# Kernel tuning notes

Hardware: AMD Instinct MI355X
Metric: run time of the kernel (lower is better)

Reference implementation:

```python
import jax, jax.numpy as jnp
import numpy as np

N_EMBD = 1024
N_HEAD = 16
B, T = 4, 2048

def setup_inputs() -> dict:
    key = jax.random.key(0)
    ks = jax.random.split(key, 5)
    s = 0.02
    return {
        "x": jax.random.normal(ks[0], (B, T, N_EMBD), dtype=jnp.float32),
        "w_attn": jax.random.normal(ks[1], (N_EMBD, 3 * N_EMBD), dtype=jnp.float32) * s,
        "b_attn": jnp.zeros((3 * N_EMBD,), dtype=jnp.float32),
        "w_proj": jax.random.normal(ks[2], (N_EMBD, N_EMBD), dtype=jnp.float32) * s,
        "b_proj": jnp.zeros((N_EMBD,), dtype=jnp.float32),
    }

def reference(x, w_attn, b_attn, w_proj, b_proj):
    Bx, Tx, C = x.shape
    hd = C // N_HEAD
    qkv = x @ w_attn + b_attn  # [B,T,3C]
    q, k, v = jnp.split(qkv, 3, axis=-1)
    # [B,H,T,hd]
    q = q.reshape(Bx, Tx, N_HEAD, hd).transpose(0, 2, 1, 3)
    k = k.reshape(Bx, Tx, N_HEAD, hd).transpose(0, 2, 1, 3)
    v = v.reshape(Bx, Tx, N_HEAD, hd).transpose(0, 2, 1, 3)
    scale = 1.0 / np.sqrt(hd).astype(np.float32)
    wei = jnp.einsum('bhqd,bhkd->bhqk', q, k) * scale
    causal = jnp.tril(jnp.ones((Tx, Tx), dtype=bool))
    wei = jnp.where(causal[None, None], wei, jnp.float32(-jnp.inf))
    wei = jax.nn.softmax(wei, axis=-1)
    out = jnp.einsum('bhqk,bhkd->bhqd', wei, v)
    out = out.transpose(0, 2, 1, 3).reshape(Bx, Tx, C)
    return out @ w_proj + b_proj
```

## Files before the change

kernel.cpp:

```cpp
#include <hip/hip_runtime.h>
#include <hip/hip_bf16.h>
#include <math.h>

#define BB 4
#define TT 2048
#define CC 1024
#define HH 16
#define HD 64
#define C3 3072
#define MM (BB * TT)

typedef __attribute__((ext_vector_type(8))) short bf16x8;
typedef __attribute__((ext_vector_type(4))) float f32x4;
typedef __attribute__((ext_vector_type(4))) short s16x4;

__device__ inline short f32_to_bf16_bits(float f) {
    unsigned u = __float_as_uint(f);
    u += 0x7fffu + ((u >> 16) & 1u);
    return (short)(u >> 16);
}

__device__ inline void async_copy16(const void* g, void* l) {
    __builtin_amdgcn_global_load_lds((const __attribute__((address_space(1))) void*)g,
                                     (__attribute__((address_space(3))) void*)l, 16, 0, 0);
}

__global__ __launch_bounds__(256) void cast_x(const float* __restrict__ in,
                                              short* __restrict__ out) {
    int i = (blockIdx.x * 256 + threadIdx.x) * 8;
    float4 a = *(const float4*)(in + i);
    float4 b = *(const float4*)(in + i + 4);
    bf16x8 o;
    o[0] = f32_to_bf16_bits(a.x); o[1] = f32_to_bf16_bits(a.y);
    o[2] = f32_to_bf16_bits(a.z); o[3] = f32_to_bf16_bits(a.w);
    o[4] = f32_to_bf16_bits(b.x); o[5] = f32_to_bf16_bits(b.y);
    o[6] = f32_to_bf16_bits(b.z); o[7] = f32_to_bf16_bits(b.w);
    *(bf16x8*)(out + i) = o;
}

__global__ __launch_bounds__(256) void tcast(const float* __restrict__ w,
                                             short* __restrict__ wt,
                                             int K, int N) {
    __shared__ short tile[64][68];
    const int n0 = blockIdx.x * 64, k0 = blockIdx.y * 64;
    const int tid = threadIdx.x;
#pragma unroll
    for (int it = 0; it < 4; ++it) {
        int idx = it * 1024 + tid * 4;
        int r = idx >> 6, c = idx & 63;
        float4 v = *(const float4*)&w[(size_t)(k0 + r) * N + n0 + c];
        tile[r][c + 0] = f32_to_bf16_bits(v.x);
        tile[r][c + 1] = f32_to_bf16_bits(v.y);
        tile[r][c + 2] = f32_to_bf16_bits(v.z);
        tile[r][c + 3] = f32_to_bf16_bits(v.w);
    }
    __syncthreads();
#pragma unroll
    for (int it = 0; it < 4; ++it) {
        int idx = it * 256 + tid;
        int rr = idx >> 4, kc = (idx & 15) * 4;
        s16x4 o = { tile[kc + 0][rr], tile[kc + 1][rr], tile[kc + 2][rr], tile[kc + 3][rr] };
        *(s16x4*)&wt[(size_t)(n0 + rr) * K + k0 + kc] = o;
    }
}

template <bool QKV>
__global__ __launch_bounds__(256) void gemm128(const short* __restrict__ A,
                                               const short* __restrict__ Bt,
                                               const float* __restrict__ bias,
                                               short* __restrict__ qb,
                                               short* __restrict__ kb,
                                               short* __restrict__ vt,
                                               float* __restrict__ out,
                                               int N, int Kdim) {
    __shared__ __align__(16) short As[128 * 64];
    __shared__ __align__(16) short Bs[128 * 64];
    const int tid = threadIdx.x;
    const int wave = tid >> 6, lane = tid & 63;
    const int quad = lane >> 4, l16 = lane & 15;
    const int wm = wave >> 1, wn = wave & 1;

    const int nbx = gridDim.x;
    const int cpc = nbx >> 3;
    const int id = blockIdx.y * nbx + blockIdx.x;
    const int cls = id & 7;
    const int rr = id >> 3;
    const int n_idx = cls * cpc + rr % cpc;
    const int m_idx = rr / cpc;
    const int m0 = m_idx * 128, n0 = n_idx * 128;

    f32x4 acc[4][4] = {};

    for (int k0 = 0; k0 < Kdim; k0 += 64) {
#pragma unroll
        for (int c2 = 0; c2 < 4; ++c2) {
            int g = (wave * 4 + c2) * 64 + lane;
            int row = g >> 3;
            int seg = (g & 7) ^ (row & 7);
            async_copy16(A + (size_t)(m0 + row) * Kdim + k0 + seg * 8, As + g * 8);
            async_copy16(Bt + (size_t)(n0 + row) * Kdim + k0 + seg * 8, Bs + g * 8);
        }
        __syncthreads();
#pragma unroll
        for (int ks = 0; ks < 2; ++ks) {
            bf16x8 af[4], bfv[4];
#pragma unroll
            for (int i = 0; i < 4; ++i) {
                int row = wm * 64 + i * 16 + l16;
                int u = (ks * 4 + quad) ^ (row & 7);
                af[i] = *(const bf16x8*)&As[row * 64 + u * 8];
            }
#pragma unroll
            for (int j = 0; j < 4; ++j) {
                int row = wn * 64 + j * 16 + l16;
                int u = (ks * 4 + quad) ^ (row & 7);
                bfv[j] = *(const bf16x8*)&Bs[row * 64 + u * 8];
            }
#pragma unroll
            for (int i = 0; i < 4; ++i)
#pragma unroll
                for (int j = 0; j < 4; ++j)
                    acc[i][j] = __builtin_amdgcn_mfma_f32_16x16x32_bf16(af[i], bfv[j], acc[i][j], 0, 0, 0);
        }
        __syncthreads();
    }

#pragma unroll
    for (int i = 0; i < 4; ++i)
#pragma unroll
        for (int j = 0; j < 4; ++j) {
            int n = n0 + wn * 64 + j * 16 + l16;
            float bv = bias[n];
            if (QKV) {
                int which = n >> 10, cc = n & 1023;
                int h = cc >> 6, d = cc & 63;
                if (which == 2) {
                    int m_base = m0 + wm * 64 + i * 16 + quad * 4;
                    int bb = m_base >> 11, t0 = m_base & 2047;
                    unsigned p0 = ((unsigned)(unsigned short)f32_to_bf16_bits(acc[i][j][0] + bv)) |
                                  ((unsigned)(unsigned short)f32_to_bf16_bits(acc[i][j][1] + bv) << 16);
                    unsigned p1 = ((unsigned)(unsigned short)f32_to_bf16_bits(acc[i][j][2] + bv)) |
                                  ((unsigned)(unsigned short)f32_to_bf16_bits(acc[i][j][3] + bv) << 16);
                    uint2 pk = {p0, p1};
                    *(uint2*)(vt + (((size_t)bb * HH + h) * HD + d) * TT + t0) = pk;
                } else {
#pragma unroll
                    for (int r = 0; r < 4; ++r) {
                        int m = m0 + wm * 64 + i * 16 + quad * 4 + r;
                        int bb = m >> 11, t = m & 2047;
                        short val = f32_to_bf16_bits((acc[i][j][r] + bv) *
                                                     (which == 0 ? 0.18033688011112042f : 1.0f));
                        size_t off = (((size_t)bb * HH + h) * TT + t) * HD + d;
                        if (which == 0) qb[off] = val;
                        else kb[off] = val;
                    }
                }
            } else {
#pragma unroll
                for (int r = 0; r < 4; ++r) {
                    int m = m0 + wm * 64 + i * 16 + quad * 4 + r;
                    out[(size_t)m * N + n] = acc[i][j][r] + bv;
                }
            }
        }
}

__global__ __launch_bounds__(512, 4) void flash_attn(const short* __restrict__ qb,
                                                     const short* __restrict__ kb,
                                                     const short* __restrict__ vt,
                                                     short* __restrict__ ab) {
    __shared__ __align__(16) short Ksh[2][4096];
    __shared__ __align__(16) short Vsh[2][4096];
    __shared__ __align__(16) float plds[8][16][68];

    const int tid = threadIdx.x;
    const int wave = tid >> 6;
    const int lane = tid & 63;
    const int quad = lane >> 4;
    const int l16 = lane & 15;

    const int n_hw = blockIdx.y * 8 + blockIdx.x;
    const int lgc = (n_hw & 7) * 64 + (n_hw >> 3);
    const int bh = lgc >> 3;
    const int i = lgc & 7;

    const int njt = 32 - 2 * i;
    const int q_lo = i * 128 + wave * 16;
    const int q_hi = (15 - i) * 128 + wave * 16;

    const short* qball = qb + (size_t)bh * TT * HD;
    const short* kball = kb + (size_t)bh * TT * HD;
    const short* vtall = vt + (size_t)bh * HD * TT;

    const int sidx = wave * 64 + lane;
    const int srow = sidx >> 3;
    const int sseg = (sidx & 7) ^ (srow & 7);
    const short* kgsrc = kball + (size_t)srow * HD + sseg * 8;
    const short* vgsrc = vtall + (size_t)srow * TT + sseg * 8;

    bf16x8 qfh[2], qfl[2];
#pragma unroll
    for (int h = 0; h < 2; ++h) {
        qfh[h] = *(const bf16x8*)(qball + (size_t)(q_hi + l16) * HD + h * 32 + quad * 8);
        qfl[h] = *(const bf16x8*)(qball + (size_t)(q_lo + l16) * HD + h * 32 + quad * 8);
    }

    f32x4 o_hi[4] = {}, o_lo[4] = {};
    float ls_hi[4] = {0.f, 0.f, 0.f, 0.f}, ls_lo[4] = {0.f, 0.f, 0.f, 0.f};

    async_copy16(kgsrc, &Ksh[0][wave * 512]);
    async_copy16(vgsrc, &Vsh[0][wave * 512]);

    for (int jt = 0; jt < njt; ++jt) {
        const int buf = jt & 1;
        if (jt + 1 < njt) {
            async_copy16(kgsrc + (size_t)(jt + 1) * 64 * HD, &Ksh[buf ^ 1][wave * 512]);
            async_copy16(vgsrc + (jt + 1) * 64, &Vsh[buf ^ 1][wave * 512]);
            asm volatile("s_waitcnt vmcnt(2)" : : : "memory");
        } else {
            asm volatile("s_waitcnt vmcnt(0)" : : : "memory");
        }
        __builtin_amdgcn_sched_barrier(0);
        __builtin_amdgcn_s_barrier();
        __builtin_amdgcn_sched_barrier(0);

        const int j0 = jt * 64;

        if (j0 <= q_hi + 15) {
            f32x4 s[4];
            __builtin_amdgcn_s_setprio(1);
#pragma unroll
            for (int cb = 0; cb < 4; ++cb) {
                int row = cb * 16 + l16;
                bf16x8 k0 = *(const bf16x8*)&Ksh[buf][(row * 8 + (quad ^ (row & 7))) * 8];
                bf16x8 k1 = *(const bf16x8*)&Ksh[buf][(row * 8 + ((4 + quad) ^ (row & 7))) * 8];
                f32x4 a = {};
                a = __builtin_amdgcn_mfma_f32_16x16x32_bf16(qfh[0], k0, a, 0, 0, 0);
                a = __builtin_amdgcn_mfma_f32_16x16x32_bf16(qfh[1], k1, a, 0, 0, 0);
                s[cb] = a;
            }
            __builtin_amdgcn_s_setprio(0);
            if (j0 + 64 > q_hi) {
#pragma unroll
                for (int cb = 0; cb < 4; ++cb) {
                    int j = j0 + cb * 16 + l16;
#pragma unroll
                    for (int r = 0; r < 4; ++r)
                        if (j > q_hi + quad * 4 + r) s[cb][r] = -1e30f;
                }
            }
#pragma unroll
            for (int cb = 0; cb < 4; ++cb)
#pragma unroll
                for (int r = 0; r < 4; ++r) {
                    float p;
                    asm("v_exp_f32 %0, %1" : "=v"(p) : "v"(s[cb][r]));
                    ls_hi[r] += p;
                    plds[wave][quad * 4 + r][cb * 16 + l16] = p;
                }
            {
                const float* prow = &plds[wave][l16][0];
                f32x4 pr0 = *(const f32x4*)(prow + quad * 8);
                f32x4 pr1 = *(const f32x4*)(prow + quad * 8 + 4);
                f32x4 pr2 = *(const f32x4*)(prow + 32 + quad * 8);
                f32x4 pr3 = *(const f32x4*)(prow + 32 + quad * 8 + 4);
                union { unsigned u[4]; bf16x8 v; } pa0u, pa1u;
                asm("v_cvt_pk_bf16_f32 %0, %1, %2" : "=v"(pa0u.u[0]) : "v"(pr0[0]), "v"(pr0[1]));
                asm("v_cvt_pk_bf16_f32 %0, %1, %2" : "=v"(pa0u.u[1]) : "v"(pr0[2]), "v"(pr0[3]));
                asm("v_cvt_pk_bf16_f32 %0, %1, %2" : "=v"(pa0u.u[2]) : "v"(pr1[0]), "v"(pr1[1]));
                asm("v_cvt_pk_bf16_f32 %0, %1, %2" : "=v"(pa0u.u[3]) : "v"(pr1[2]), "v"(pr1[3]));
                asm("v_cvt_pk_bf16_f32 %0, %1, %2" : "=v"(pa1u.u[0]) : "v"(pr2[0]), "v"(pr2[1]));
                asm("v_cvt_pk_bf16_f32 %0, %1, %2" : "=v"(pa1u.u[1]) : "v"(pr2[2]), "v"(pr2[3]));
                asm("v_cvt_pk_bf16_f32 %0, %1, %2" : "=v"(pa1u.u[2]) : "v"(pr3[0]), "v"(pr3[1]));
                asm("v_cvt_pk_bf16_f32 %0, %1, %2" : "=v"(pa1u.u[3]) : "v"(pr3[2]), "v"(pr3[3]));
                bf16x8 pa0 = pa0u.v, pa1 = pa1u.v;
                __builtin_amdgcn_s_setprio(1);
#pragma unroll
                for (int db = 0; db < 4; ++db) {
                    int row = db * 16 + l16;
                    bf16x8 v0 = *(const bf16x8*)&Vsh[buf][(row * 8 + (quad ^ (row & 7))) * 8];
                    bf16x8 v1 = *(const bf16x8*)&Vsh[buf][(row * 8 + ((4 + quad) ^ (row & 7))) * 8];
                    o_hi[db] = __builtin_amdgcn_mfma_f32_16x16x32_bf16(pa0, v0, o_hi[db], 0, 0, 0);
                    o_hi[db] = __builtin_amdgcn_mfma_f32_16x16x32_bf16(pa1, v1, o_hi[db], 0, 0, 0);
                }
                __builtin_amdgcn_s_setprio(0);
            }
        }

        if (j0 <= q_lo + 15) {
            f32x4 s[4];
            __builtin_amdgcn_s_setprio(1);
#pragma unroll
            for (int cb = 0; cb < 4; ++cb) {
                int row = cb * 16 + l16;
                bf16x8 k0 = *(const bf16x8*)&Ksh[buf][(row * 8 + (quad ^ (row & 7))) * 8];
                bf16x8 k1 = *(const bf16x8*)&Ksh[buf][(row * 8 + ((4 + quad) ^ (row & 7))) * 8];
                f32x4 a = {};
                a = __builtin_amdgcn_mfma_f32_16x16x32_bf16(qfl[0], k0, a, 0, 0, 0);
                a = __builtin_amdgcn_mfma_f32_16x16x32_bf16(qfl[1], k1, a, 0, 0, 0);
                s[cb] = a;
            }
            __builtin_amdgcn_s_setprio(0);
            if (j0 + 64 > q_lo) {
#pragma unroll
                for (int cb = 0; cb < 4; ++cb) {
                    int j = j0 + cb * 16 + l16;
#pragma unroll
                    for (int r = 0; r < 4; ++r)
                        if (j > q_lo + quad * 4 + r) s[cb][r] = -1e30f;
                }
            }
#pragma unroll
            for (int cb = 0; cb < 4; ++cb)
#pragma unroll
                for (int r = 0; r < 4; ++r) {
                    float p;
                    asm("v_exp_f32 %0, %1" : "=v"(p) : "v"(s[cb][r]));
                    ls_lo[r] += p;
                    plds[wave][quad * 4 + r][cb * 16 + l16] = p;
                }
            {
                const float* prow = &plds[wave][l16][0];
                f32x4 pr0 = *(const f32x4*)(prow + quad * 8);
                f32x4 pr1 = *(const f32x4*)(prow + quad * 8 + 4);
                f32x4 pr2 = *(const f32x4*)(prow + 32 + quad * 8);
                f32x4 pr3 = *(const f32x4*)(prow + 32 + quad * 8 + 4);
                union { unsigned u[4]; bf16x8 v; } pa0u, pa1u;
                asm("v_cvt_pk_bf16_f32 %0, %1, %2" : "=v"(pa0u.u[0]) : "v"(pr0[0]), "v"(pr0[1]));
                asm("v_cvt_pk_bf16_f32 %0, %1, %2" : "=v"(pa0u.u[1]) : "v"(pr0[2]), "v"(pr0[3]));
                asm("v_cvt_pk_bf16_f32 %0, %1, %2" : "=v"(pa0u.u[2]) : "v"(pr1[0]), "v"(pr1[1]));
                asm("v_cvt_pk_bf16_f32 %0, %1, %2" : "=v"(pa0u.u[3]) : "v"(pr1[2]), "v"(pr1[3]));
                asm("v_cvt_pk_bf16_f32 %0, %1, %2" : "=v"(pa1u.u[0]) : "v"(pr2[0]), "v"(pr2[1]));
                asm("v_cvt_pk_bf16_f32 %0, %1, %2" : "=v"(pa1u.u[1]) : "v"(pr2[2]), "v"(pr2[3]));
                asm("v_cvt_pk_bf16_f32 %0, %1, %2" : "=v"(pa1u.u[2]) : "v"(pr3[0]), "v"(pr3[1]));
                asm("v_cvt_pk_bf16_f32 %0, %1, %2" : "=v"(pa1u.u[3]) : "v"(pr3[2]), "v"(pr3[3]));
                bf16x8 pa0 = pa0u.v, pa1 = pa1u.v;
                __builtin_amdgcn_s_setprio(1);
#pragma unroll
                for (int db = 0; db < 4; ++db) {
                    int row = db * 16 + l16;
                    bf16x8 v0 = *(const bf16x8*)&Vsh[buf][(row * 8 + (quad ^ (row & 7))) * 8];
                    bf16x8 v1 = *(const bf16x8*)&Vsh[buf][(row * 8 + ((4 + quad) ^ (row & 7))) * 8];
                    o_lo[db] = __builtin_amdgcn_mfma_f32_16x16x32_bf16(pa0, v0, o_lo[db], 0, 0, 0);
                    o_lo[db] = __builtin_amdgcn_mfma_f32_16x16x32_bf16(pa1, v1, o_lo[db], 0, 0, 0);
                }
                __builtin_amdgcn_s_setprio(0);
            }
        }
        __builtin_amdgcn_sched_barrier(0);
        __builtin_amdgcn_s_barrier();
    }

    const int b = bh >> 4, hd0 = (bh & 15) * HD;
    float inv_h[4], inv_l[4];
#pragma unroll
    for (int r = 0; r < 4; ++r) {
        float th = ls_hi[r], tl = ls_lo[r];
#pragma unroll
        for (int off = 1; off < 16; off <<= 1) {
            th += __shfl_xor(th, off, 64);
            tl += __shfl_xor(tl, off, 64);
        }
        inv_h[r] = 1.0f / th;
        inv_l[r] = 1.0f / tl;
    }
#pragma unroll
    for (int r = 0; r < 4; ++r) {
        int qh = q_hi + quad * 4 + r;
        int ql = q_lo + quad * 4 + r;
#pragma unroll
        for (int db = 0; db < 4; ++db) {
            ab[((size_t)(b * TT + qh)) * CC + hd0 + db * 16 + l16] =
                f32_to_bf16_bits(o_hi[db][r] * inv_h[r]);
            ab[((size_t)(b * TT + ql)) * CC + hd0 + db * 16 + l16] =
                f32_to_bf16_bits(o_lo[db][r] * inv_l[r]);
        }
    }
}

extern "C" void kernel_launch(void* const* d_in, const int* in_sizes, int n_in,
                              void* d_out, int out_size, void* d_ws, size_t ws_size,
                              hipStream_t stream) {
    const float* x      = (const float*)d_in[0];
    const float* w_attn = (const float*)d_in[1];
    const float* b_attn = (const float*)d_in[2];
    const float* w_proj = (const float*)d_in[3];
    const float* b_proj = (const float*)d_in[4];
    float* out = (float*)d_out;

    const size_t per = (size_t)BB * HH * TT * HD;
    short* xb      = (short*)d_ws;
    short* wt_attn = xb + per;
    short* wt_proj = wt_attn + (size_t)C3 * CC;
    short* qb      = wt_proj + (size_t)CC * CC;
    short* kb      = qb + per;
    short* vt      = kb + per;
    short* ab      = vt + per;

    cast_x<<<dim3(MM * CC / (256 * 8)), 256, 0, stream>>>(x, xb);
    tcast<<<dim3(C3 / 64, CC / 64), 256, 0, stream>>>(w_attn, wt_attn, CC, C3);
    tcast<<<dim3(CC / 64, CC / 64), 256, 0, stream>>>(w_proj, wt_proj, CC, CC);

    gemm128<true><<<dim3(C3 / 128, MM / 128), 256, 0, stream>>>(
        xb, wt_attn, b_attn, qb, kb, vt, nullptr, C3, CC);

    flash_attn<<<dim3(8, BB * HH), 512, 0, stream>>>(qb, kb, vt, ab);

    gemm128<false><<<dim3(CC / 128, MM / 128), 256, 0, stream>>>(
        ab, wt_proj, b_proj, nullptr, nullptr, nullptr, out, CC, CC);
}
```

Baseline: 165.7 us.

## Triple-buffer K/V tiles with one barrier per step and bf16 P staging

Switches the K/V shared-memory staging from double to triple buffering. Loads are now issued two tiles ahead, right after the barrier, which allows the trailing per-iteration barrier to be dropped so each step has a single synchronization. Probabilities are also converted to bf16 before being written to LDS, so the P operands come back with a single 16-byte read per half instead of float loads plus packing. The cost is more LDS per block, which may reduce occupancy, and the correctness of the one-barrier buffer rotation needs care.

```diff
diff --git a/kernel.cpp b/kernel.cpp
--- a/kernel.cpp
+++ b/kernel.cpp
@@ -169,9 +169,9 @@
                                                      const short* __restrict__ kb,
                                                      const short* __restrict__ vt,
                                                      short* __restrict__ ab) {
-    __shared__ __align__(16) short Ksh[2][4096];
-    __shared__ __align__(16) short Vsh[2][4096];
-    __shared__ __align__(16) float plds[8][16][68];
+    __shared__ __align__(16) short Ksh[3][4096];
+    __shared__ __align__(16) short Vsh[3][4096];
+    __shared__ __align__(16) short plds[8][16][72];
 
     const int tid = threadIdx.x;
     const int wave = tid >> 6;
@@ -210,19 +210,21 @@
 
     async_copy16(kgsrc, &Ksh[0][wave * 512]);
     async_copy16(vgsrc, &Vsh[0][wave * 512]);
-
+    async_copy16(kgsrc + (size_t)64 * HD, &Ksh[1][wave * 512]);
+    async_copy16(vgsrc + 64, &Vsh[1][wave * 512]);
+
+    int buf = 0;
     for (int jt = 0; jt < njt; ++jt) {
-        const int buf = jt & 1;
-        if (jt + 1 < njt) {
-            async_copy16(kgsrc + (size_t)(jt + 1) * 64 * HD, &Ksh[buf ^ 1][wave * 512]);
-            async_copy16(vgsrc + (jt + 1) * 64, &Vsh[buf ^ 1][wave * 512]);
-            asm volatile("s_waitcnt vmcnt(2)" : : : "memory");
-        } else {
-            asm volatile("s_waitcnt vmcnt(0)" : : : "memory");
-        }
+        if (jt == njt - 1) { asm volatile("s_waitcnt vmcnt(0)" : : : "memory"); }
+        else               { asm volatile("s_waitcnt vmcnt(2)" : : : "memory"); }
         __builtin_amdgcn_sched_barrier(0);
         __builtin_amdgcn_s_barrier();
         __builtin_amdgcn_sched_barrier(0);
+        if (jt + 2 < njt) {
+            int pbuf = (buf >= 1) ? buf - 1 : 2;
+            async_copy16(kgsrc + (size_t)(jt + 2) * 64 * HD, &Ksh[pbuf][wave * 512]);
+            async_copy16(vgsrc + (jt + 2) * 64, &Vsh[pbuf][wave * 512]);
+        }
 
         const int j0 = jt * 64;
 
@@ -256,24 +258,13 @@
                     float p;
                     asm("v_exp_f32 %0, %1" : "=v"(p) : "v"(s[cb][r]));
                     ls_hi[r] += p;
-                    plds[wave][quad * 4 + r][cb * 16 + l16] = p;
+                    unsigned pk;
+                    asm("v_cvt_pk_bf16_f32 %0, %1, %2" : "=v"(pk) : "v"(p), "v"(p));
+                    plds[wave][quad * 4 + r][cb * 16 + l16] = (short)pk;
                 }
             {
-                const float* prow = &plds[wave][l16][0];
-                f32x4 pr0 = *(const f32x4*)(prow + quad * 8);
-                f32x4 pr1 = *(const f32x4*)(prow + quad * 8 + 4);
-                f32x4 pr2 = *(const f32x4*)(prow + 32 + quad * 8);
-                f32x4 pr3 = *(const f32x4*)(prow + 32 + quad * 8 + 4);
-                union { unsigned u[4]; bf16x8 v; } pa0u, pa1u;
-                asm("v_cvt_pk_bf16_f32 %0, %1, %2" : "=v"(pa0u.u[0]) : "v"(pr0[0]), "v"(pr0[1]));
-                asm("v_cvt_pk_bf16_f32 %0, %1, %2" : "=v"(pa0u.u[1]) : "v"(pr0[2]), "v"(pr0[3]));
-                asm("v_cvt_pk_bf16_f32 %0, %1, %2" : "=v"(pa0u.u[2]) : "v"(pr1[0]), "v"(pr1[1]));
-                asm("v_cvt_pk_bf16_f32 %0, %1, %2" : "=v"(pa0u.u[3]) : "v"(pr1[2]), "v"(pr1[3]));
-                asm("v_cvt_pk_bf16_f32 %0, %1, %2" : "=v"(pa1u.u[0]) : "v"(pr2[0]), "v"(pr2[1]));
-                asm("v_cvt_pk_bf16_f32 %0, %1, %2" : "=v"(pa1u.u[1]) : "v"(pr2[2]), "v"(pr2[3]));
-                asm("v_cvt_pk_bf16_f32 %0, %1, %2" : "=v"(pa1u.u[2]) : "v"(pr3[0]), "v"(pr3[1]));
-                asm("v_cvt_pk_bf16_f32 %0, %1, %2" : "=v"(pa1u.u[3]) : "v"(pr3[2]), "v"(pr3[3]));
-                bf16x8 pa0 = pa0u.v, pa1 = pa1u.v;
+                bf16x8 pa0 = *(const bf16x8*)&plds[wave][l16][quad * 8];
+                bf16x8 pa1 = *(const bf16x8*)&plds[wave][l16][32 + quad * 8];
                 __builtin_amdgcn_s_setprio(1);
 #pragma unroll
                 for (int db = 0; db < 4; ++db) {
@@ -317,24 +308,13 @@
                     float p;
                     asm("v_exp_f32 %0, %1" : "=v"(p) : "v"(s[cb][r]));
                     ls_lo[r] += p;
-                    plds[wave][quad * 4 + r][cb * 16 + l16] = p;
+                    unsigned pk;
+                    asm("v_cvt_pk_bf16_f32 %0, %1, %2" : "=v"(pk) : "v"(p), "v"(p));
+                    plds[wave][quad * 4 + r][cb * 16 + l16] = (short)pk;
                 }
             {
-                const float* prow = &plds[wave][l16][0];
-                f32x4 pr0 = *(const f32x4*)(prow + quad * 8);
-                f32x4 pr1 = *(const f32x4*)(prow + quad * 8 + 4);
-                f32x4 pr2 = *(const f32x4*)(prow + 32 + quad * 8);
-                f32x4 pr3 = *(const f32x4*)(prow + 32 + quad * 8 + 4);
-                union { unsigned u[4]; bf16x8 v; } pa0u, pa1u;
-                asm("v_cvt_pk_bf16_f32 %0, %1, %2" : "=v"(pa0u.u[0]) : "v"(pr0[0]), "v"(pr0[1]));
-                asm("v_cvt_pk_bf16_f32 %0, %1, %2" : "=v"(pa0u.u[1]) : "v"(pr0[2]), "v"(pr0[3]));
-                asm("v_cvt_pk_bf16_f32 %0, %1, %2" : "=v"(pa0u.u[2]) : "v"(pr1[0]), "v"(pr1[1]));
-                asm("v_cvt_pk_bf16_f32 %0, %1, %2" : "=v"(pa0u.u[3]) : "v"(pr1[2]), "v"(pr1[3]));
-                asm("v_cvt_pk_bf16_f32 %0, %1, %2" : "=v"(pa1u.u[0]) : "v"(pr2[0]), "v"(pr2[1]));
-                asm("v_cvt_pk_bf16_f32 %0, %1, %2" : "=v"(pa1u.u[1]) : "v"(pr2[2]), "v"(pr2[3]));
-                asm("v_cvt_pk_bf16_f32 %0, %1, %2" : "=v"(pa1u.u[2]) : "v"(pr3[0]), "v"(pr3[1]));
-                asm("v_cvt_pk_bf16_f32 %0, %1, %2" : "=v"(pa1u.u[3]) : "v"(pr3[2]), "v"(pr3[3]));
-                bf16x8 pa0 = pa0u.v, pa1 = pa1u.v;
+                bf16x8 pa0 = *(const bf16x8*)&plds[wave][l16][quad * 8];
+                bf16x8 pa1 = *(const bf16x8*)&plds[wave][l16][32 + quad * 8];
                 __builtin_amdgcn_s_setprio(1);
 #pragma unroll
                 for (int db = 0; db < 4; ++db) {
@@ -347,8 +327,7 @@
                 __builtin_amdgcn_s_setprio(0);
             }
         }
-        __builtin_amdgcn_sched_barrier(0);
-        __builtin_amdgcn_s_barrier();
+        buf = (buf == 2) ? 0 : buf + 1;
     }
 
     const int b = bh >> 4, hd0 = (bh & 15) * HD;
```

Measured after the change: 166.9 us. No clear change (+0.7%).
